# Kernel optimization log

Hardware: AMD Instinct MI355X
Metric: run time of the kernel (lower is better)

Reference implementation:

```python
import jax, jax.numpy as jnp
import numpy as np

N_ENTITIES = 4096
FEATURE_DIM = 512
CELLS = 39
PAIRS = 8192


def setup_inputs() -> dict:
    key = jax.random.key(0)
    k_emb, k_idx, k_wg, k_wl = jax.random.split(key, 4)
    embedding = jax.random.normal(k_emb, (N_ENTITIES, FEATURE_DIM), dtype=jnp.float32)
    index = jax.random.randint(k_idx, (CELLS, PAIRS, 2), 0, N_ENTITIES, dtype=jnp.int32)
    # kaiming_uniform-style scale for the global bilinear weight
    bound_g = np.sqrt(6.0 / FEATURE_DIM)
    weights_global = jax.random.uniform(k_wg, (FEATURE_DIM, FEATURE_DIM), minval=-bound_g, maxval=bound_g, dtype=jnp.float32)
    # per-cell diagonal scaling vectors (original stores them as [d,1] params)
    weights_local = jax.random.uniform(k_wl, (CELLS, FEATURE_DIM), minval=-bound_g, maxval=bound_g, dtype=jnp.float32)
    return {"embedding": embedding, "index": index,
            "weights_global": weights_global, "weights_local": weights_local}


def reference(embedding, index, weights_global, weights_local):
    # Original per-cell math: einsum('bn,nm,mj,jk,bk->b', A, diag(wl), W, diag(wl), B)
    # diag(wl) @ ... is just elementwise scaling of the gathered embeddings, so:
    #   out[c,p] = sum_{n,k} (A[c,p,n]*wl[c,n]) * W[n,k] * (B[c,p,k]*wl[c,k])
    wl = weights_local[:, None, :]                      # [C,1,d]
    A = embedding[index[..., 0]] * wl                   # [C,P,d]
    B = embedding[index[..., 1]] * wl                   # [C,P,d]
    return jnp.einsum('cpn,nk,cpk->cp', A, weights_global, B)  # [C,P]
```

## Files before the change

kernel.cpp:

```cpp
#include <hip/hip_runtime.h>
#include <stdint.h>

#define NE 4096
#define FD 512
#define NCELLS 39
#define NPAIRS 8192

typedef __attribute__((ext_vector_type(8))) short short8;
typedef __attribute__((ext_vector_type(8))) unsigned short ushort8;
typedef __attribute__((ext_vector_type(4))) float f32x4;
typedef __attribute__((ext_vector_type(4))) unsigned int uint4v;

__device__ __forceinline__ unsigned short f2bf(float f) {
  union { float f; uint32_t u; } v; v.f = f;
  uint32_t u = v.u;
  return (unsigned short)((u + 0x7fffu + ((u >> 16) & 1u)) >> 16);
}
__device__ __forceinline__ float bf2f(unsigned short b) {
  return __uint_as_float(((uint32_t)b) << 16);
}

__device__ __forceinline__ void async16(const void* g, void* l) {
  __builtin_amdgcn_global_load_lds((const __attribute__((address_space(1))) void*)g,
                                   (__attribute__((address_space(3))) void*)l, 16, 0, 0);
}

__global__ __launch_bounds__(256) void conv_e(const float* __restrict__ E,
                                              unsigned short* __restrict__ Ebf) {
  const int i = blockIdx.x * 256 + threadIdx.x;
  const float4 v = ((const float4*)E)[i];
  ushort4 o;
  o.x = f2bf(v.x); o.y = f2bf(v.y); o.z = f2bf(v.z); o.w = f2bf(v.w);
  ((ushort4*)Ebf)[i] = o;
}

__global__ __launch_bounds__(256) void prep_w(const float* __restrict__ W,
                                              const float* __restrict__ wl,
                                              unsigned short* __restrict__ Wt,
                                              int c0) {
  __shared__ float tile[32][33];
  const int ci = blockIdx.z;
  const int tn = blockIdx.x * 32, tk = blockIdx.y * 32;
  const int tx = threadIdx.x & 31, ty = threadIdx.x >> 5;
  const float* wlr = wl + (size_t)(c0 + ci) * FD;
#pragma unroll
  for (int i = 0; i < 4; i++) {
    int n = tn + ty + i * 8;
    tile[ty + i * 8][tx] = W[(size_t)n * FD + tk + tx] * wlr[n];
  }
  __syncthreads();
  unsigned short* dst = Wt + (size_t)ci * FD * FD;
#pragma unroll
  for (int i = 0; i < 4; i++) {
    int kout = tk + ty + i * 8;
    dst[(size_t)kout * FD + tn + tx] = f2bf(tile[tx][ty + i * 8] * wlr[kout]);
  }
}

__global__ __launch_bounds__(256) void gemm_k(const unsigned short* __restrict__ Ebf,
                                              const unsigned short* __restrict__ Wt,
                                              unsigned short* __restrict__ U) {
  __shared__ unsigned short As[128 * 32];
  __shared__ unsigned short Bs[128 * 32];
  const int t = threadIdx.x;
  const int ci = blockIdx.z;
  const unsigned short* Ag = Ebf + (size_t)blockIdx.x * 128 * FD;
  const unsigned short* Bg = Wt + (size_t)ci * FD * FD + (size_t)blockIdx.y * 128 * FD;

  f32x4 acc[4][4];
#pragma unroll
  for (int i = 0; i < 4; i++)
#pragma unroll
    for (int j = 0; j < 4; j++) acc[i][j] = (f32x4){0.f, 0.f, 0.f, 0.f};

  const int wave = t >> 6, lane = t & 63;
  const int wm = (wave & 1) * 64, wn = (wave >> 1) * 64;
  const int lr = lane & 15, lq = lane >> 4;
  const int idx0 = t, idx1 = 256 + t;
  const int r0 = idx0 >> 2, cb0 = (idx0 & 3) * 8;
  const int r1 = idx1 >> 2, cb1 = (idx1 & 3) * 8;

  for (int k0 = 0; k0 < FD; k0 += 32) {
    async16(Ag + (size_t)r0 * FD + k0 + cb0, &As[idx0 * 8]);
    async16(Ag + (size_t)r1 * FD + k0 + cb1, &As[idx1 * 8]);
    async16(Bg + (size_t)r0 * FD + k0 + cb0, &Bs[idx0 * 8]);
    async16(Bg + (size_t)r1 * FD + k0 + cb1, &Bs[idx1 * 8]);
    __syncthreads();
    short8 af[4], bq[4];
#pragma unroll
    for (int mi = 0; mi < 4; mi++) af[mi] = *(const short8*)&As[(wm + mi * 16 + lr) * 32 + lq * 8];
#pragma unroll
    for (int ni = 0; ni < 4; ni++) bq[ni] = *(const short8*)&Bs[(wn + ni * 16 + lr) * 32 + lq * 8];
#pragma unroll
    for (int mi = 0; mi < 4; mi++)
#pragma unroll
      for (int ni = 0; ni < 4; ni++)
        acc[mi][ni] = __builtin_amdgcn_mfma_f32_16x16x32_bf16(af[mi], bq[ni], acc[mi][ni], 0, 0, 0);
    __syncthreads();
  }

  unsigned short* Up = U + (size_t)ci * NE * FD;
#pragma unroll
  for (int mi = 0; mi < 4; mi++) {
    int mbase = blockIdx.x * 128 + wm + mi * 16 + lq * 4;
#pragma unroll
    for (int ni = 0; ni < 4; ni++) {
      int n = blockIdx.y * 128 + wn + ni * 16 + lr;
#pragma unroll
      for (int r = 0; r < 4; r++) {
        Up[(size_t)(mbase + r) * FD + n] = f2bf(acc[mi][ni][r]);
      }
    }
  }
}

__global__ __launch_bounds__(256) void dot_k(const unsigned short* __restrict__ U,
                                             const unsigned short* __restrict__ Ebf,
                                             const int* __restrict__ index,
                                             float* __restrict__ out,
                                             int c0) {
  const int ci = blockIdx.y;
  const int c = c0 + ci;
  const int wave = threadIdx.x >> 6, lane = threadIdx.x & 63;
  const unsigned short* Uc = U + (size_t)ci * NE * FD;
  const size_t cp = (size_t)c * NPAIRS;
  const int2* idx2 = (const int2*)index + cp;
  float* op = out + cp;
  const int pbase = (blockIdx.x * 4 + wave) * 32;

  for (int batch = 0; batch < 4; batch++) {
    const int pb = pbase + batch * 8;
    int2 id[8];
#pragma unroll
    for (int b = 0; b < 8; b++) id[b] = idx2[pb + b];
    uint4v uv[8], ev[8];
#pragma unroll
    for (int b = 0; b < 8; b++) {
      uv[b] = __builtin_nontemporal_load((const uint4v*)(Uc + (size_t)id[b].x * FD + lane * 8));
      ev[b] = *(const uint4v*)(Ebf + (size_t)id[b].y * FD + lane * 8);
    }
#pragma unroll
    for (int b = 0; b < 8; b++) {
      const ushort8 u = *(const ushort8*)&uv[b];
      const ushort8 e = *(const ushort8*)&ev[b];
      float s = 0.f;
#pragma unroll
      for (int q = 0; q < 8; q++) s += bf2f(u[q]) * bf2f(e[q]);
      s += __shfl_xor(s, 1, 64);
      s += __shfl_xor(s, 2, 64);
      s += __shfl_xor(s, 4, 64);
      s += __shfl_xor(s, 8, 64);
      s += __shfl_xor(s, 16, 64);
      s += __shfl_xor(s, 32, 64);
      if (lane == b) op[pb + b] = s;
    }
  }
}

__global__ __launch_bounds__(256) void naive_k(const float* __restrict__ emb,
                                               const int* __restrict__ index,
                                               const float* __restrict__ W,
                                               const float* __restrict__ wl,
                                               float* __restrict__ out) {
  __shared__ float bs[FD];
  __shared__ float red[256];
  const int c = blockIdx.y, p = blockIdx.x;
  const int i0 = index[((size_t)c * NPAIRS + p) * 2];
  const int i1 = index[((size_t)c * NPAIRS + p) * 2 + 1];
  const float* wlc = wl + (size_t)c * FD;
  for (int k = threadIdx.x; k < FD; k += 256) bs[k] = emb[(size_t)i1 * FD + k] * wlc[k];
  __syncthreads();
  float s = 0.f;
  for (int n = threadIdx.x; n < FD; n += 256) {
    const float* wr = W + (size_t)n * FD;
    float tacc = 0.f;
    for (int k = 0; k < FD; k++) tacc += wr[k] * bs[k];
    s += tacc * emb[(size_t)i0 * FD + n] * wlc[n];
  }
  red[threadIdx.x] = s;
  __syncthreads();
  for (int st = 128; st > 0; st >>= 1) {
    if (threadIdx.x < st) red[threadIdx.x] += red[threadIdx.x + st];
    __syncthreads();
  }
  if (threadIdx.x == 0) out[(size_t)c * NPAIRS + p] = red[0];
}

extern "C" void kernel_launch(void* const* d_in, const int* in_sizes, int n_in,
                              void* d_out, int out_size, void* d_ws, size_t ws_size,
                              hipStream_t stream) {
  const float* emb = (const float*)d_in[0];
  const int* index = (const int*)d_in[1];
  const float* Wg = (const float*)d_in[2];
  const float* wl = (const float*)d_in[3];
  float* out = (float*)d_out;

  const size_t ebytes = (size_t)NE * FD * 2;
  const size_t wtcell = (size_t)FD * FD * 2;
  const size_t ucell = (size_t)NE * FD * 2;
  size_t avail = ws_size > ebytes ? ws_size - ebytes : 0;
  int G = (int)(avail / (wtcell + ucell));
  if (G > NCELLS) G = NCELLS;

  if (G < 1) {
    naive_k<<<dim3(NPAIRS, NCELLS), 256, 0, stream>>>(emb, index, Wg, wl, out);
    return;
  }

  unsigned short* Ebf = (unsigned short*)d_ws;
  unsigned short* Wt = (unsigned short*)((char*)d_ws + ebytes);
  unsigned short* U = (unsigned short*)((char*)d_ws + ebytes + (size_t)G * wtcell);

  conv_e<<<dim3((NE * FD / 4) / 256), 256, 0, stream>>>(emb, Ebf);
  for (int c0 = 0; c0 < NCELLS; c0 += G) {
    int g = (NCELLS - c0 < G) ? (NCELLS - c0) : G;
    prep_w<<<dim3(FD / 32, FD / 32, g), 256, 0, stream>>>(Wg, wl, Wt, c0);
    gemm_k<<<dim3(NE / 128, FD / 128, g), 256, 0, stream>>>(Ebf, Wt, U);
    dot_k<<<dim3(NPAIRS / 128, g), 256, 0, stream>>>(U, Ebf, index, out, c0);
  }
}
```

Measured before the change: 243.7 us.

## Bucket pairs by left index and stage U rows in LDS for dot

Adds a per-cell bucketing kernel that sorts pair indices into 64 buckets by the left entity row and packs pair id, right index and local row into one word. The dot kernel then loads a 64-row slice of U into shared memory once per block and serves the left-operand reads from LDS, so each pair only gathers the right embedding row from global memory. This is meant to remove the random global gathers of U rows. It costs an extra launch plus atomics, a 64KB LDS footprint per block that limits occupancy, and unbalanced bucket sizes across blocks.

```diff
diff --git a/kernel.cpp b/kernel.cpp
--- a/kernel.cpp
+++ b/kernel.cpp
@@ -57,6 +57,36 @@
   }
 }
 
+__global__ __launch_bounds__(256) void bucket_k(const int* __restrict__ index,
+                                                uint32_t* __restrict__ buckets,
+                                                int* __restrict__ offs) {
+  __shared__ int hist[64];
+  __shared__ int base[64];
+  __shared__ int cur[64];
+  const int ci = blockIdx.x;
+  const int t = threadIdx.x;
+  if (t < 64) hist[t] = 0;
+  __syncthreads();
+  const int2* idx = (const int2*)index + (size_t)ci * NPAIRS;
+  for (int j = t; j < NPAIRS; j += 256) {
+    int2 id = idx[j];
+    atomicAdd(&hist[id.x >> 6], 1);
+  }
+  __syncthreads();
+  if (t == 0) {
+    int s = 0;
+    for (int b = 0; b < 64; b++) { base[b] = s; cur[b] = s; s += hist[b]; }
+  }
+  __syncthreads();
+  if (t < 64) offs[ci * 64 + t] = base[t];
+  for (int j = t; j < NPAIRS; j += 256) {
+    int2 id = idx[j];
+    int pos = atomicAdd(&cur[id.x >> 6], 1);
+    buckets[(size_t)ci * NPAIRS + pos] =
+        (uint32_t)j | ((uint32_t)id.y << 13) | ((uint32_t)(id.x & 63) << 25);
+  }
+}
+
 __global__ __launch_bounds__(256) void gemm_k(const unsigned short* __restrict__ Ebf,
                                               const unsigned short* __restrict__ Wt,
                                               unsigned short* __restrict__ U) {
@@ -114,45 +144,55 @@
   }
 }
 
-__global__ __launch_bounds__(256) void dot_k(const unsigned short* __restrict__ U,
+__global__ __launch_bounds__(256) void dot_b(const unsigned short* __restrict__ U,
                                              const unsigned short* __restrict__ Ebf,
-                                             const int* __restrict__ index,
+                                             const uint32_t* __restrict__ buckets,
+                                             const int* __restrict__ offs,
                                              float* __restrict__ out,
                                              int c0) {
-  const int ci = blockIdx.y;
-  const int c = c0 + ci;
-  const int wave = threadIdx.x >> 6, lane = threadIdx.x & 63;
-  const unsigned short* Uc = U + (size_t)ci * NE * FD;
-  const size_t cp = (size_t)c * NPAIRS;
-  const int2* idx2 = (const int2*)index + cp;
-  float* op = out + cp;
-  const int pbase = (blockIdx.x * 4 + wave) * 32;
-
-  for (int batch = 0; batch < 4; batch++) {
-    const int pb = pbase + batch * 8;
-    int2 id[8];
-#pragma unroll
-    for (int b = 0; b < 8; b++) id[b] = idx2[pb + b];
-    uint4v uv[8], ev[8];
+  __shared__ __align__(16) unsigned short Ul[64 * FD];
+  const int ci = blockIdx.y, bx = blockIdx.x;
+  const int t = threadIdx.x;
+  const int wave = t >> 6, lane = t & 63;
+
+  const unsigned short* Uw = U + ((size_t)ci * NE + (size_t)bx * 64) * FD;
+#pragma unroll
+  for (int pass = 0; pass < 16; pass++)
+    async16(Uw + pass * 2048 + t * 8, &Ul[pass * 2048 + t * 8]);
+  __syncthreads();
+
+  const int cg = c0 + ci;
+  const int off0 = offs[cg * 64 + bx];
+  const int off1 = (bx == 63) ? NPAIRS : offs[cg * 64 + bx + 1];
+  const uint32_t* bk = buckets + (size_t)cg * NPAIRS;
+  float* op = out + (size_t)cg * NPAIRS;
+
+  for (int j = off0 + wave * 8; j < off1; j += 32) {
+    const int m = off1 - j;
+    uint32_t w[8];
+#pragma unroll
+    for (int b = 0; b < 8; b++) w[b] = bk[j + (b < m ? b : 0)];
+    uint4v ev[8];
+#pragma unroll
+    for (int b = 0; b < 8; b++)
+      ev[b] = *(const uint4v*)(Ebf + (size_t)((w[b] >> 13) & 0xFFF) * FD + lane * 8);
+    ushort8 uu[8];
+#pragma unroll
+    for (int b = 0; b < 8; b++)
+      uu[b] = *(const ushort8*)&Ul[(w[b] >> 25) * FD + lane * 8];
 #pragma unroll
     for (int b = 0; b < 8; b++) {
-      uv[b] = __builtin_nontemporal_load((const uint4v*)(Uc + (size_t)id[b].x * FD + lane * 8));
-      ev[b] = *(const uint4v*)(Ebf + (size_t)id[b].y * FD + lane * 8);
-    }
-#pragma unroll
-    for (int b = 0; b < 8; b++) {
-      const ushort8 u = *(const ushort8*)&uv[b];
       const ushort8 e = *(const ushort8*)&ev[b];
       float s = 0.f;
 #pragma unroll
-      for (int q = 0; q < 8; q++) s += bf2f(u[q]) * bf2f(e[q]);
+      for (int q = 0; q < 8; q++) s += bf2f(uu[b][q]) * bf2f(e[q]);
       s += __shfl_xor(s, 1, 64);
       s += __shfl_xor(s, 2, 64);
       s += __shfl_xor(s, 4, 64);
       s += __shfl_xor(s, 8, 64);
       s += __shfl_xor(s, 16, 64);
       s += __shfl_xor(s, 32, 64);
-      if (lane == b) op[pb + b] = s;
+      if (lane == 0 && b < m) op[w[b] & 0x1FFF] = s;
     }
   }
 }
@@ -196,9 +236,12 @@
   float* out = (float*)d_out;
 
   const size_t ebytes = (size_t)NE * FD * 2;
+  const size_t bbytes = (size_t)NCELLS * NPAIRS * 4;
+  const size_t obytes = (size_t)NCELLS * 64 * 4;
   const size_t wtcell = (size_t)FD * FD * 2;
   const size_t ucell = (size_t)NE * FD * 2;
-  size_t avail = ws_size > ebytes ? ws_size - ebytes : 0;
+  const size_t fixed = ebytes + bbytes + obytes;
+  size_t avail = ws_size > fixed ? ws_size - fixed : 0;
   int G = (int)(avail / (wtcell + ucell));
   if (G > NCELLS) G = NCELLS;
 
@@ -208,14 +251,17 @@
   }
 
   unsigned short* Ebf = (unsigned short*)d_ws;
-  unsigned short* Wt = (unsigned short*)((char*)d_ws + ebytes);
-  unsigned short* U = (unsigned short*)((char*)d_ws + ebytes + (size_t)G * wtcell);
+  uint32_t* buckets = (uint32_t*)((char*)d_ws + ebytes);
+  int* offs = (int*)((char*)d_ws + ebytes + bbytes);
+  unsigned short* Wt = (unsigned short*)((char*)d_ws + fixed);
+  unsigned short* U = (unsigned short*)((char*)d_ws + fixed + (size_t)G * wtcell);
 
   conv_e<<<dim3((NE * FD / 4) / 256), 256, 0, stream>>>(emb, Ebf);
+  bucket_k<<<dim3(NCELLS), 256, 0, stream>>>(index, buckets, offs);
   for (int c0 = 0; c0 < NCELLS; c0 += G) {
     int g = (NCELLS - c0 < G) ? (NCELLS - c0) : G;
     prep_w<<<dim3(FD / 32, FD / 32, g), 256, 0, stream>>>(Wg, wl, Wt, c0);
     gemm_k<<<dim3(NE / 128, FD / 128, g), 256, 0, stream>>>(Ebf, Wt, U);
-    dot_k<<<dim3(NPAIRS / 128, g), 256, 0, stream>>>(U, Ebf, index, out, c0);
-  }
-}
+    dot_b<<<dim3(64, g), 256, 0, stream>>>(U, Ebf, buckets, offs, out, c0);
+  }
+}
```

Result: slower. 275.5 us (+13.0%).

## Bucket pairs by first index to localize U row gathers in dot kernel

Applied to the files above, without the earlier changes.

Adds a per-cell counting-sort kernel that reorders pairs into 64 buckets keyed on the first entity index, packing the original position and second index into a descriptor. The dot kernel then walks pairs in bucket order, so the U-row gathers within a block and across nearby blocks touch a narrower range of U and should get better cache locality, and results are scattered back to their original positions. This adds an extra launch, extra workspace for the descriptors, and scattered output writes.

```diff
diff --git a/kernel.cpp b/kernel.cpp
--- a/kernel.cpp
+++ b/kernel.cpp
@@ -57,6 +57,33 @@
   }
 }
 
+__global__ __launch_bounds__(256) void bucket_k(const int* __restrict__ index,
+                                                uint2* __restrict__ dsc) {
+  __shared__ int hist[64];
+  __shared__ int cur[64];
+  const int ci = blockIdx.x;
+  const int t = threadIdx.x;
+  if (t < 64) hist[t] = 0;
+  __syncthreads();
+  const int2* idx = (const int2*)index + (size_t)ci * NPAIRS;
+  for (int j = t; j < NPAIRS; j += 256) {
+    int2 id = idx[j];
+    atomicAdd(&hist[id.x >> 6], 1);
+  }
+  __syncthreads();
+  if (t == 0) {
+    int s = 0;
+    for (int b = 0; b < 64; b++) { cur[b] = s; s += hist[b]; }
+  }
+  __syncthreads();
+  uint2* dc = dsc + (size_t)ci * NPAIRS;
+  for (int j = t; j < NPAIRS; j += 256) {
+    int2 id = idx[j];
+    int pos = atomicAdd(&cur[id.x >> 6], 1);
+    dc[pos] = make_uint2((uint32_t)j | ((uint32_t)id.y << 13), (uint32_t)id.x);
+  }
+}
+
 __global__ __launch_bounds__(256) void gemm_k(const unsigned short* __restrict__ Ebf,
                                               const unsigned short* __restrict__ Wt,
                                               unsigned short* __restrict__ U) {
@@ -114,30 +141,29 @@
   }
 }
 
-__global__ __launch_bounds__(256) void dot_k(const unsigned short* __restrict__ U,
+__global__ __launch_bounds__(256) void dot_s(const unsigned short* __restrict__ U,
                                              const unsigned short* __restrict__ Ebf,
-                                             const int* __restrict__ index,
+                                             const uint2* __restrict__ dsc,
                                              float* __restrict__ out,
                                              int c0) {
   const int ci = blockIdx.y;
-  const int c = c0 + ci;
+  const int cg = c0 + ci;
   const int wave = threadIdx.x >> 6, lane = threadIdx.x & 63;
   const unsigned short* Uc = U + (size_t)ci * NE * FD;
-  const size_t cp = (size_t)c * NPAIRS;
-  const int2* idx2 = (const int2*)index + cp;
-  float* op = out + cp;
-  const int pbase = (blockIdx.x * 4 + wave) * 32;
+  const uint2* dc = dsc + (size_t)cg * NPAIRS;
+  float* op = out + (size_t)cg * NPAIRS;
+  const int jbase = blockIdx.x * 128 + wave * 32;
 
   for (int batch = 0; batch < 4; batch++) {
-    const int pb = pbase + batch * 8;
-    int2 id[8];
-#pragma unroll
-    for (int b = 0; b < 8; b++) id[b] = idx2[pb + b];
+    const int jb = jbase + batch * 8;
+    uint2 d[8];
+#pragma unroll
+    for (int b = 0; b < 8; b++) d[b] = dc[jb + b];
     uint4v uv[8], ev[8];
 #pragma unroll
     for (int b = 0; b < 8; b++) {
-      uv[b] = __builtin_nontemporal_load((const uint4v*)(Uc + (size_t)id[b].x * FD + lane * 8));
-      ev[b] = *(const uint4v*)(Ebf + (size_t)id[b].y * FD + lane * 8);
+      uv[b] = __builtin_nontemporal_load((const uint4v*)(Uc + (size_t)d[b].y * FD + lane * 8));
+      ev[b] = *(const uint4v*)(Ebf + (size_t)((d[b].x >> 13) & 0xFFF) * FD + lane * 8);
     }
 #pragma unroll
     for (int b = 0; b < 8; b++) {
@@ -152,7 +178,7 @@
       s += __shfl_xor(s, 8, 64);
       s += __shfl_xor(s, 16, 64);
       s += __shfl_xor(s, 32, 64);
-      if (lane == b) op[pb + b] = s;
+      if (lane == b) op[d[b].x & 0x1FFF] = s;
     }
   }
 }
@@ -196,9 +222,11 @@
   float* out = (float*)d_out;
 
   const size_t ebytes = (size_t)NE * FD * 2;
+  const size_t dbytes = (size_t)NCELLS * NPAIRS * 8;
   const size_t wtcell = (size_t)FD * FD * 2;
   const size_t ucell = (size_t)NE * FD * 2;
-  size_t avail = ws_size > ebytes ? ws_size - ebytes : 0;
+  const size_t fixed = ebytes + dbytes;
+  size_t avail = ws_size > fixed ? ws_size - fixed : 0;
   int G = (int)(avail / (wtcell + ucell));
   if (G > NCELLS) G = NCELLS;
 
@@ -208,14 +236,16 @@
   }
 
   unsigned short* Ebf = (unsigned short*)d_ws;
-  unsigned short* Wt = (unsigned short*)((char*)d_ws + ebytes);
-  unsigned short* U = (unsigned short*)((char*)d_ws + ebytes + (size_t)G * wtcell);
+  uint2* dsc = (uint2*)((char*)d_ws + ebytes);
+  unsigned short* Wt = (unsigned short*)((char*)d_ws + fixed);
+  unsigned short* U = (unsigned short*)((char*)d_ws + fixed + (size_t)G * wtcell);
 
   conv_e<<<dim3((NE * FD / 4) / 256), 256, 0, stream>>>(emb, Ebf);
+  bucket_k<<<dim3(NCELLS), 256, 0, stream>>>(index, dsc);
   for (int c0 = 0; c0 < NCELLS; c0 += G) {
     int g = (NCELLS - c0 < G) ? (NCELLS - c0) : G;
     prep_w<<<dim3(FD / 32, FD / 32, g), 256, 0, stream>>>(Wg, wl, Wt, c0);
     gemm_k<<<dim3(NE / 128, FD / 128, g), 256, 0, stream>>>(Ebf, Wt, U);
-    dot_k<<<dim3(NPAIRS / 128, g), 256, 0, stream>>>(U, Ebf, index, out, c0);
-  }
-}
+    dot_s<<<dim3(NPAIRS / 128, g), 256, 0, stream>>>(U, Ebf, dsc, out, c0);
+  }
+}
```

After: 263.4 us. +8.1%, slower.
